# Kernel tuning notes

Measured on AMD Instinct MI355X. Metric: run time of the kernel, lower is better.

The kernel has to match this reference:

```python
import jax, jax.numpy as jnp
import numpy as np

B, F, S, H = 1024, 64, 512, 128


def setup_inputs() -> dict:
    key = jax.random.key(0)
    ks = jax.random.split(key, 9)
    x = jax.random.normal(ks[0], (B, F, S), dtype=jnp.float32)
    available_len = jax.random.randint(ks[1], (B,), 1, S // 2).astype(jnp.int32)
    extra = jax.random.randint(ks[2], (B,), 0, S // 2)
    predict_len = jnp.minimum(available_len + extra, S).astype(jnp.int32)
    s = 1.0 / float(np.sqrt(H))  # PyTorch default uniform init scale
    u = lambda k, shape: jax.random.uniform(k, shape, jnp.float32, -s, s)
    W_ih = u(ks[3], (4 * H, F))
    W_hh = u(ks[4], (4 * H, H))
    b_ih = u(ks[5], (4 * H,))
    b_hh = u(ks[6], (4 * H,))
    W_den = u(ks[7], (F, H))
    b_den = u(ks[8], (F,))
    init_ch = jnp.zeros((1, 2 * H), dtype=jnp.float32)  # nn.Parameter(zeros(1, 2*n_hidden))
    return {"x": x, "available_len": available_len, "predict_len": predict_len,
            "W_ih": W_ih, "W_hh": W_hh, "b_ih": b_ih, "b_hh": b_hh,
            "W_den": W_den, "b_den": b_den, "init_ch": init_ch}


def reference(x, available_len, predict_len, W_ih, W_hh, b_ih, b_hh, W_den, b_den, init_ch):
    """Masked autoregressive LSTMCell recurrence.

    Row r is active at step t iff t < predict_len[r]; once inactive it never
    re-activates (the torch code's per-step gather of c_1/h_1 by predict_len is
    exactly this monotone-shrinking active set, expressed here as a masked
    full-batch state update). For t >= available_len[r] (and still active) the
    input is the model's own previous prediction (auto-regression feedback).
    Returns the permuted buffer (seq_len, batch, n_fea), matching the torch code.
    """
    Bb, Ff, Ss = x.shape
    Hh = W_hh.shape[1]
    xs = jnp.transpose(x, (2, 0, 1))  # (S, B, F)
    c0 = jnp.broadcast_to(init_ch[:, :Hh], (Bb, Hh))
    h0 = jnp.broadcast_to(init_ch[:, Hh:], (Bb, Hh))

    def step(carry, inp):
        h, c, prev_out = carry
        t, x_t = inp  # t: scalar step index, x_t: (B, F)
        sel = t < predict_len                       # active rows
        use_pred = (t >= available_len) & sel
        inp_t = jnp.where(use_pred[:, None], prev_out, x_t)
        gates = inp_t @ W_ih.T + b_ih + h @ W_hh.T + b_hh  # (B, 4H)
        i, f, g, o = jnp.split(gates, 4, axis=-1)
        c_new = jax.nn.sigmoid(f) * c + jax.nn.sigmoid(i) * jnp.tanh(g)
        h_new = jax.nn.sigmoid(o) * jnp.tanh(c_new)
        h = jnp.where(sel[:, None], h_new, h)
        c = jnp.where(sel[:, None], c_new, c)
        pred = h_new @ W_den.T + b_den              # (B, F)
        out_t = jnp.where(sel[:, None], pred, inp_t)  # x[t, sel] <- prediction
        return (h, c, out_t), out_t

    _, ys = jax.lax.scan(step, (h0, c0, jnp.zeros_like(xs[0])),
                         (jnp.arange(Ss), xs))
    return ys  # (S, B, F)
```

## Files before the change

kernel.cpp:

```cpp
#include <hip/hip_runtime.h>

#define BB 1024
#define FF 64
#define SS 512
#define HH 128
#define ZP 200
#define ZROWS 16
#define OUTS (BB*FF)

typedef __attribute__((ext_vector_type(8))) short bf16x8;
typedef __attribute__((ext_vector_type(4))) float f32x4;

__device__ __forceinline__ unsigned short f2bf(float f) {
    unsigned int u = __float_as_uint(f);
    u += 0x7fff + ((u >> 16) & 1);
    return (unsigned short)(u >> 16);
}

__device__ __forceinline__ void bar_lds() {
    __builtin_amdgcn_sched_barrier(0);
    asm volatile("s_waitcnt lgkmcnt(0)\n\ts_barrier" ::: "memory");
    __builtin_amdgcn_sched_barrier(0);
}

__global__ void fold_kernel(const float* __restrict__ W_ih,
                            const float* __restrict__ W_den,
                            const float* __restrict__ b_den,
                            float* __restrict__ ws)
{
    const int n = blockIdx.x;
    const int k = threadIdx.x;
    float s = 0.f;
    #pragma unroll 8
    for (int f = 0; f < FF; ++f) s = fmaf(W_ih[n*FF + f], W_den[f*HH + k], s);
    ws[n*HH + k] = s;
    if (k == 0) {
        float bsum = 0.f;
        #pragma unroll 8
        for (int f = 0; f < FF; ++f) bsum = fmaf(W_ih[n*FF + f], b_den[f], bsum);
        ws[4*HH*HH + n] = bsum;
    }
}

__global__ __launch_bounds__(512)
void lstm_mfma_kernel(const float* __restrict__ x,
                      const int* __restrict__ available_len,
                      const int* __restrict__ predict_len,
                      const float* __restrict__ W_ih,
                      const float* __restrict__ W_hh,
                      const float* __restrict__ b_ih,
                      const float* __restrict__ b_hh,
                      const float* __restrict__ W_den,
                      const float* __restrict__ b_den,
                      const float* __restrict__ init_ch,
                      const float* __restrict__ ws,
                      float* __restrict__ out)
{
    const int b0  = blockIdx.x * 4;
    const int tid = threadIdx.x;
    const int w   = tid >> 6;
    const int l   = tid & 63;
    const int l16 = l & 15;
    const int lq  = l >> 4;
    const bool w4 = (w < 4);

    __shared__ __align__(16) unsigned short zbuf[2][ZROWS * ZP];

    for (int i = tid; i < 2 * ZROWS * ZP / 2; i += 512)
        ((unsigned int*)zbuf)[i] = 0u;

    const int p0 = predict_len[b0], p1 = predict_len[b0+1],
              p2 = predict_len[b0+2], p3 = predict_len[b0+3];
    const int a0i = available_len[b0], a1i = available_len[b0+1],
              a2i = available_len[b0+2], a3i = available_len[b0+3];
    const int maxP  = max(max(p0, p1), max(p2, p3));
    const int tsw   = max(max(a0i, a1i), max(a2i, a3i));
    const int P_my  = predict_len[b0 + lq];
    const int AV_my = available_len[b0 + lq];

    bf16x8 wg[4][6];
    float bias[4];
    #pragma unroll
    for (int g = 0; g < 4; ++g) {
        const int n = 128*g + 16*w + l16;
        const float* rih = W_ih + n * FF;
        const float* rhh = W_hh + n * HH;
        #pragma unroll
        for (int kt = 0; kt < 6; ++kt) {
            const int k = 32*kt + 8*lq;
            const float* src = (k < 64) ? (rih + k) : (rhh + (k - 64));
            bf16x8 r;
            #pragma unroll
            for (int i = 0; i < 8; i++) r[i] = (short)f2bf(src[i]);
            wg[g][kt] = r;
        }
        bias[g] = b_ih[n] + b_hh[n];
    }

    bf16x8 wd0, wd1, wd2, wd3;
    float bden = 0.f;
    size_t xbase = 0;
    int AV_x = 0;
    if (w4) {
        const int f = 16*w + l16;
        const float* rd = W_den + f * HH;
        bf16x8 r;
        #pragma unroll
        for (int i = 0; i < 8; i++) r[i] = (short)f2bf(rd[0*32 + 8*lq + i]);
        wd0 = r;
        #pragma unroll
        for (int i = 0; i < 8; i++) r[i] = (short)f2bf(rd[1*32 + 8*lq + i]);
        wd1 = r;
        #pragma unroll
        for (int i = 0; i < 8; i++) r[i] = (short)f2bf(rd[2*32 + 8*lq + i]);
        wd2 = r;
        #pragma unroll
        for (int i = 0; i < 8; i++) r[i] = (short)f2bf(rd[3*32 + 8*lq + i]);
        wd3 = r;
        bden = b_den[f];
        xbase = ((size_t)(b0 + w) * FF + l) * SS;
        AV_x  = available_len[b0 + w];
    }

    const int unit  = 16*w + l16;
    const int abase = l16*ZP + 8*lq;
    float c = init_ch[unit];
    const float h0v = init_ch[HH + unit];
    float* outb = out + (size_t)(b0 + lq) * FF + 16*w + l16;

    bar_lds();

    zbuf[0][(4*lq)*ZP + 64 + unit] = f2bf(h0v);
    if (w4) zbuf[0][(4*w)*ZP + l] = f2bf(x[xbase]);

    float4 qc = {0.f,0.f,0.f,0.f};
    if (w4 && AV_x > 1) qc = *(const float4*)(x + xbase);

    int cur = 0;

#define DO_STEP(S, XNEXT)                                                      \
  do {                                                                         \
    const int s_ = (S);                                                        \
    bar_lds();                                               \
    const unsigned short* zc_ = zbuf[cur];                                     \
    bf16x8 a0 = *(const bf16x8*)(zc_ + abase +   0);                           \
    bf16x8 a1 = *(const bf16x8*)(zc_ + abase +  32);                           \
    bf16x8 a2 = *(const bf16x8*)(zc_ + abase +  64);                           \
    bf16x8 a3 = *(const bf16x8*)(zc_ + abase +  96);                           \
    bf16x8 a4 = *(const bf16x8*)(zc_ + abase + 128);                           \
    bf16x8 a5 = *(const bf16x8*)(zc_ + abase + 160);                           \
    f32x4 ac0 = {0.f,0.f,0.f,0.f}, ac1 = {0.f,0.f,0.f,0.f},                    \
          ac2 = {0.f,0.f,0.f,0.f}, ac3 = {0.f,0.f,0.f,0.f};                    \
    ac0 = __builtin_amdgcn_mfma_f32_16x16x32_bf16(a0, wg[0][0], ac0, 0,0,0);   \
    ac1 = __builtin_amdgcn_mfma_f32_16x16x32_bf16(a0, wg[1][0], ac1, 0,0,0);   \
    ac2 = __builtin_amdgcn_mfma_f32_16x16x32_bf16(a0, wg[2][0], ac2, 0,0,0);   \
    ac3 = __builtin_amdgcn_mfma_f32_16x16x32_bf16(a0, wg[3][0], ac3, 0,0,0);   \
    ac0 = __builtin_amdgcn_mfma_f32_16x16x32_bf16(a1, wg[0][1], ac0, 0,0,0);   \
    ac1 = __builtin_amdgcn_mfma_f32_16x16x32_bf16(a1, wg[1][1], ac1, 0,0,0);   \
    ac2 = __builtin_amdgcn_mfma_f32_16x16x32_bf16(a1, wg[2][1], ac2, 0,0,0);   \
    ac3 = __builtin_amdgcn_mfma_f32_16x16x32_bf16(a1, wg[3][1], ac3, 0,0,0);   \
    ac0 = __builtin_amdgcn_mfma_f32_16x16x32_bf16(a2, wg[0][2], ac0, 0,0,0);   \
    ac1 = __builtin_amdgcn_mfma_f32_16x16x32_bf16(a2, wg[1][2], ac1, 0,0,0);   \
    ac2 = __builtin_amdgcn_mfma_f32_16x16x32_bf16(a2, wg[2][2], ac2, 0,0,0);   \
    ac3 = __builtin_amdgcn_mfma_f32_16x16x32_bf16(a2, wg[3][2], ac3, 0,0,0);   \
    ac0 = __builtin_amdgcn_mfma_f32_16x16x32_bf16(a3, wg[0][3], ac0, 0,0,0);   \
    ac1 = __builtin_amdgcn_mfma_f32_16x16x32_bf16(a3, wg[1][3], ac1, 0,0,0);   \
    ac2 = __builtin_amdgcn_mfma_f32_16x16x32_bf16(a3, wg[2][3], ac2, 0,0,0);   \
    ac3 = __builtin_amdgcn_mfma_f32_16x16x32_bf16(a3, wg[3][3], ac3, 0,0,0);   \
    ac0 = __builtin_amdgcn_mfma_f32_16x16x32_bf16(a4, wg[0][4], ac0, 0,0,0);   \
    ac1 = __builtin_amdgcn_mfma_f32_16x16x32_bf16(a4, wg[1][4], ac1, 0,0,0);   \
    ac2 = __builtin_amdgcn_mfma_f32_16x16x32_bf16(a4, wg[2][4], ac2, 0,0,0);   \
    ac3 = __builtin_amdgcn_mfma_f32_16x16x32_bf16(a4, wg[3][4], ac3, 0,0,0);   \
    ac0 = __builtin_amdgcn_mfma_f32_16x16x32_bf16(a5, wg[0][5], ac0, 0,0,0);   \
    ac1 = __builtin_amdgcn_mfma_f32_16x16x32_bf16(a5, wg[1][5], ac1, 0,0,0);   \
    ac2 = __builtin_amdgcn_mfma_f32_16x16x32_bf16(a5, wg[2][5], ac2, 0,0,0);   \
    ac3 = __builtin_amdgcn_mfma_f32_16x16x32_bf16(a5, wg[3][5], ac3, 0,0,0);   \
    const float g0 = ac0[0] + bias[0];                                         \
    const float g1 = ac1[0] + bias[1];                                         \
    const float g2 = ac2[0] + bias[2];                                         \
    const float g3 = ac3[0] + bias[3];                                         \
    const float si = 1.f / (1.f + __expf(-g0));                                \
    const float sf = 1.f / (1.f + __expf(-g1));                                \
    const float tg = 1.f - 2.f / (__expf(2.f * g2) + 1.f);                     \
    const float so = 1.f / (1.f + __expf(-g3));                                \
    const float cn = sf * c + si * tg;                                         \
    const float tc = 1.f - 2.f / (__expf(2.f * cn) + 1.f);                     \
    const float hn = so * tc;                                                  \
    const int nxt_ = cur ^ 1;                                                  \
    if (s_ < P_my) { c = cn; zbuf[nxt_][(4*lq)*ZP + 64 + unit] = f2bf(hn); }   \
    bar_lds();                                                \
    if (w4) {                                                                  \
      const unsigned short* zn_ = zbuf[nxt_];                                  \
      bf16x8 h0f = *(const bf16x8*)(zn_ + abase + 64 +  0);                    \
      bf16x8 h1f = *(const bf16x8*)(zn_ + abase + 64 + 32);                    \
      bf16x8 h2f = *(const bf16x8*)(zn_ + abase + 64 + 64);                    \
      bf16x8 h3f = *(const bf16x8*)(zn_ + abase + 64 + 96);                    \
      f32x4 pa = {0.f,0.f,0.f,0.f}, pb = {0.f,0.f,0.f,0.f};                    \
      pa = __builtin_amdgcn_mfma_f32_16x16x32_bf16(h0f, wd0, pa, 0,0,0);       \
      pb = __builtin_amdgcn_mfma_f32_16x16x32_bf16(h2f, wd2, pb, 0,0,0);       \
      pa = __builtin_amdgcn_mfma_f32_16x16x32_bf16(h1f, wd1, pa, 0,0,0);       \
      pb = __builtin_amdgcn_mfma_f32_16x16x32_bf16(h3f, wd3, pb, 0,0,0);       \
      const float pred_ = pa[0] + pb[0] + bden;                                \
      if (s_ < P_my) {                                                         \
        outb[(size_t)s_ * OUTS] = pred_;                                       \
        if (s_ + 1 >= AV_my)                                                   \
          zbuf[nxt_][(4*lq)*ZP + 16*w + l16] = f2bf(pred_);                    \
      }                                                                        \
      if (s_ + 1 < AV_x) zbuf[nxt_][(4*w)*ZP + l] = f2bf(XNEXT);               \
    }                                                                          \
    cur = nxt_;                                                                \
  } while (0)

    int t4 = 0;
    for (; t4 + 4 <= tsw; t4 += 4) {
        float4 qn = {0.f,0.f,0.f,0.f};
        if (w4 && (t4 + 4 < AV_x))
            qn = *(const float4*)(x + xbase + t4 + 4);
        DO_STEP(t4 + 0, qc.y);
        DO_STEP(t4 + 1, qc.z);
        DO_STEP(t4 + 2, qc.w);
        DO_STEP(t4 + 3, qn.x);
        qc = qn;
    }
    for (; t4 < tsw; ++t4) {
        float xs = 0.f;
        if (w4 && (t4 + 1 < AV_x)) xs = x[xbase + t4 + 1];
        DO_STEP(t4, xs);
    }
#undef DO_STEP

    if (tsw < maxP) {
        const float* wfold = ws;
        const float* bfold = ws + 4*HH*HH;
        #pragma unroll
        for (int g = 0; g < 4; ++g) {
            const int n = 128*g + 16*w + l16;
            const float* rhh = W_hh + n * HH;
            const float* rfo = wfold + n * HH;
            #pragma unroll
            for (int j = 0; j < 4; ++j) {
                const int k = 32*j + 8*lq;
                bf16x8 r;
                #pragma unroll
                for (int i = 0; i < 8; i++) r[i] = (short)f2bf(rhh[k+i] + rfo[k+i]);
                wg[g][j] = r;
            }
            bias[g] += bfold[n];
        }

        for (int t = tsw; t < maxP; ++t) {
            bar_lds();
            const unsigned short* zc = zbuf[cur];
            bf16x8 h0f = *(const bf16x8*)(zc + abase + 64 +  0);
            bf16x8 h1f = *(const bf16x8*)(zc + abase + 64 + 32);
            bf16x8 h2f = *(const bf16x8*)(zc + abase + 64 + 64);
            bf16x8 h3f = *(const bf16x8*)(zc + abase + 64 + 96);

            if (w4) {
                f32x4 pa = {0.f,0.f,0.f,0.f}, pb = {0.f,0.f,0.f,0.f};
                pa = __builtin_amdgcn_mfma_f32_16x16x32_bf16(h0f, wd0, pa, 0,0,0);
                pb = __builtin_amdgcn_mfma_f32_16x16x32_bf16(h2f, wd2, pb, 0,0,0);
                pa = __builtin_amdgcn_mfma_f32_16x16x32_bf16(h1f, wd1, pa, 0,0,0);
                pb = __builtin_amdgcn_mfma_f32_16x16x32_bf16(h3f, wd3, pb, 0,0,0);
                if (t > tsw && (t - 1) < P_my)
                    outb[(size_t)(t-1) * OUTS] = pa[0] + pb[0] + bden;
            }

            f32x4 ac0 = {0.f,0.f,0.f,0.f}, ac1 = {0.f,0.f,0.f,0.f},
                  ac2 = {0.f,0.f,0.f,0.f}, ac3 = {0.f,0.f,0.f,0.f};
            ac0 = __builtin_amdgcn_mfma_f32_16x16x32_bf16(h0f, wg[0][0], ac0, 0,0,0);
            ac1 = __builtin_amdgcn_mfma_f32_16x16x32_bf16(h0f, wg[1][0], ac1, 0,0,0);
            ac2 = __builtin_amdgcn_mfma_f32_16x16x32_bf16(h0f, wg[2][0], ac2, 0,0,0);
            ac3 = __builtin_amdgcn_mfma_f32_16x16x32_bf16(h0f, wg[3][0], ac3, 0,0,0);
            ac0 = __builtin_amdgcn_mfma_f32_16x16x32_bf16(h1f, wg[0][1], ac0, 0,0,0);
            ac1 = __builtin_amdgcn_mfma_f32_16x16x32_bf16(h1f, wg[1][1], ac1, 0,0,0);
            ac2 = __builtin_amdgcn_mfma_f32_16x16x32_bf16(h1f, wg[2][1], ac2, 0,0,0);
            ac3 = __builtin_amdgcn_mfma_f32_16x16x32_bf16(h1f, wg[3][1], ac3, 0,0,0);
            ac0 = __builtin_amdgcn_mfma_f32_16x16x32_bf16(h2f, wg[0][2], ac0, 0,0,0);
            ac1 = __builtin_amdgcn_mfma_f32_16x16x32_bf16(h2f, wg[1][2], ac1, 0,0,0);
            ac2 = __builtin_amdgcn_mfma_f32_16x16x32_bf16(h2f, wg[2][2], ac2, 0,0,0);
            ac3 = __builtin_amdgcn_mfma_f32_16x16x32_bf16(h2f, wg[3][2], ac3, 0,0,0);
            ac0 = __builtin_amdgcn_mfma_f32_16x16x32_bf16(h3f, wg[0][3], ac0, 0,0,0);
            ac1 = __builtin_amdgcn_mfma_f32_16x16x32_bf16(h3f, wg[1][3], ac1, 0,0,0);
            ac2 = __builtin_amdgcn_mfma_f32_16x16x32_bf16(h3f, wg[2][3], ac2, 0,0,0);
            ac3 = __builtin_amdgcn_mfma_f32_16x16x32_bf16(h3f, wg[3][3], ac3, 0,0,0);

            const float g0 = ac0[0] + bias[0];
            const float g1 = ac1[0] + bias[1];
            const float g2 = ac2[0] + bias[2];
            const float g3 = ac3[0] + bias[3];
            const float si = 1.f / (1.f + __expf(-g0));
            const float sf = 1.f / (1.f + __expf(-g1));
            const float tg = 1.f - 2.f / (__expf(2.f * g2) + 1.f);
            const float so = 1.f / (1.f + __expf(-g3));
            const float cn = sf * c + si * tg;
            const float tc = 1.f - 2.f / (__expf(2.f * cn) + 1.f);
            const float hn = so * tc;

            const int nxt = cur ^ 1;
            if (t < P_my) { c = cn; zbuf[nxt][(4*lq)*ZP + 64 + unit] = f2bf(hn); }
            cur = nxt;
        }

        bar_lds();
        if (w4) {
            const unsigned short* zc = zbuf[cur];
            bf16x8 h0f = *(const bf16x8*)(zc + abase + 64 +  0);
            bf16x8 h1f = *(const bf16x8*)(zc + abase + 64 + 32);
            bf16x8 h2f = *(const bf16x8*)(zc + abase + 64 + 64);
            bf16x8 h3f = *(const bf16x8*)(zc + abase + 64 + 96);
            f32x4 pa = {0.f,0.f,0.f,0.f}, pb = {0.f,0.f,0.f,0.f};
            pa = __builtin_amdgcn_mfma_f32_16x16x32_bf16(h0f, wd0, pa, 0,0,0);
            pb = __builtin_amdgcn_mfma_f32_16x16x32_bf16(h2f, wd2, pb, 0,0,0);
            pa = __builtin_amdgcn_mfma_f32_16x16x32_bf16(h1f, wd1, pa, 0,0,0);
            pb = __builtin_amdgcn_mfma_f32_16x16x32_bf16(h3f, wd3, pb, 0,0,0);
            if ((maxP - 1) < P_my)
                outb[(size_t)(maxP-1) * OUTS] = pa[0] + pb[0] + bden;
        }
    }
}

__global__ void tail_copy(const float* __restrict__ x,
                          const int* __restrict__ predict_len,
                          float* __restrict__ out)
{
    __shared__ float tile[64][65];
    const int b  = blockIdx.x;
    const int t0 = blockIdx.y * 64;
    const int P  = predict_len[b];
    if (t0 + 64 <= P) return;

    const int tid = threadIdx.x;
    const int tt  = tid & 63;
    const int fb  = tid >> 6;
    #pragma unroll
    for (int i = 0; i < 16; i++) {
        int f = fb * 16 + i;
        tile[f][tt] = x[(size_t)b * FF * SS + (size_t)f * SS + t0 + tt];
    }
    __syncthreads();
    const int f2 = tid & 63;
    const int tb = tid >> 6;
    #pragma unroll
    for (int i = 0; i < 16; i++) {
        int tloc = tb * 16 + i;
        int t    = t0 + tloc;
        if (t >= P) out[(size_t)t * BB * FF + (size_t)b * FF + f2] = tile[f2][tloc];
    }
}

extern "C" void kernel_launch(void* const* d_in, const int* in_sizes, int n_in,
                              void* d_out, int out_size, void* d_ws, size_t ws_size,
                              hipStream_t stream) {
    const float* x       = (const float*)d_in[0];
    const int*   avail   = (const int*)  d_in[1];
    const int*   plen    = (const int*)  d_in[2];
    const float* W_ih    = (const float*)d_in[3];
    const float* W_hh    = (const float*)d_in[4];
    const float* b_ih    = (const float*)d_in[5];
    const float* b_hh    = (const float*)d_in[6];
    const float* W_den   = (const float*)d_in[7];
    const float* b_den   = (const float*)d_in[8];
    const float* init_ch = (const float*)d_in[9];
    float*       out     = (float*)d_out;
    float*       ws      = (float*)d_ws;

    fold_kernel<<<dim3(4*HH), dim3(HH), 0, stream>>>(W_ih, W_den, b_den, ws);
    tail_copy<<<dim3(BB, SS/64), dim3(256), 0, stream>>>(x, plen, out);
    lstm_mfma_kernel<<<dim3(BB/4), dim3(512), 0, stream>>>(
        x, avail, plen, W_ih, W_hh, b_ih, b_hh, W_den, b_den, init_ch, ws, out);
}
```

Baseline: 444.9 us.

## Sort batch rows by available length so blocks group similar-length sequences

A new single-block kernel ranks rows by available_len to build a permutation. The LSTM kernel then handles 4 permuted rows per block, so each block's teacher-forced phase (up to max available_len) and its autoregressive phase line up more tightly and fewer masked steps are wasted. Prediction outputs are now written during the teacher-forced steps as well, through dense-projection MFMAs fused into each step. This adds a serial O(B^2) sort kernel, indirect row indexing and extra MFMAs per step in exchange for lower per-block step counts.

Measured after the change: 472.6 us. +6.2%, slower.

```diff
diff --git a/kernel.cpp b/kernel.cpp
--- a/kernel.cpp
+++ b/kernel.cpp
@@ -42,6 +42,18 @@
     }
 }
 
+__global__ void sort_kernel(const int* __restrict__ avail, int* __restrict__ perm)
+{
+    const int i = threadIdx.x;
+    const int key = avail[i];
+    int rank = 0;
+    for (int j = 0; j < BB; ++j) {
+        const int kj = avail[j];
+        rank += (kj < key) || (kj == key && j < i);
+    }
+    perm[rank] = i;
+}
+
 __global__ __launch_bounds__(512)
 void lstm_mfma_kernel(const float* __restrict__ x,
                       const int* __restrict__ available_len,
@@ -54,6 +66,7 @@
                       const float* __restrict__ b_den,
                       const float* __restrict__ init_ch,
                       const float* __restrict__ ws,
+                      const int* __restrict__ perm,
                       float* __restrict__ out)
 {
     const int b0  = blockIdx.x * 4;
@@ -69,14 +82,18 @@
     for (int i = tid; i < 2 * ZROWS * ZP / 2; i += 512)
         ((unsigned int*)zbuf)[i] = 0u;
 
-    const int p0 = predict_len[b0], p1 = predict_len[b0+1],
-              p2 = predict_len[b0+2], p3 = predict_len[b0+3];
-    const int a0i = available_len[b0], a1i = available_len[b0+1],
-              a2i = available_len[b0+2], a3i = available_len[b0+3];
+    const int rr0 = perm[b0], rr1 = perm[b0+1], rr2 = perm[b0+2], rr3 = perm[b0+3];
+    const int p0 = predict_len[rr0], p1 = predict_len[rr1],
+              p2 = predict_len[rr2], p3 = predict_len[rr3];
+    const int a0i = available_len[rr0], a1i = available_len[rr1],
+              a2i = available_len[rr2], a3i = available_len[rr3];
     const int maxP  = max(max(p0, p1), max(p2, p3));
     const int tsw   = max(max(a0i, a1i), max(a2i, a3i));
-    const int P_my  = predict_len[b0 + lq];
-    const int AV_my = available_len[b0 + lq];
+    const int tmin  = min(min(a0i, a1i), min(a2i, a3i));
+    const int ph1s  = (tmin > 1) ? (tmin - 1) : 0;
+    const int rl    = perm[b0 + lq];
+    const int P_my  = predict_len[rl];
+    const int AV_my = available_len[rl];
 
     bf16x8 wg[4][6];
     float bias[4];
@@ -118,15 +135,16 @@
         for (int i = 0; i < 8; i++) r[i] = (short)f2bf(rd[3*32 + 8*lq + i]);
         wd3 = r;
         bden = b_den[f];
-        xbase = ((size_t)(b0 + w) * FF + l) * SS;
-        AV_x  = available_len[b0 + w];
+        const int rx = perm[b0 + w];
+        xbase = ((size_t)rx * FF + l) * SS;
+        AV_x  = available_len[rx];
     }
 
     const int unit  = 16*w + l16;
     const int abase = l16*ZP + 8*lq;
     float c = init_ch[unit];
     const float h0v = init_ch[HH + unit];
-    float* outb = out + (size_t)(b0 + lq) * FF + 16*w + l16;
+    float* outb = out + (size_t)rl * FF + 16*w + l16;
 
     bar_lds();
 
@@ -134,9 +152,71 @@
     if (w4) zbuf[0][(4*w)*ZP + l] = f2bf(x[xbase]);
 
     float4 qc = {0.f,0.f,0.f,0.f};
-    if (w4 && AV_x > 1) qc = *(const float4*)(x + xbase);
+    if (AV_x > 1) qc = *(const float4*)(x + xbase);
 
     int cur = 0;
+
+#define DO_T(S, XNEXT)                                                         \
+  do {                                                                         \
+    const int s_ = (S);                                                        \
+    bar_lds();                                             \
+    const unsigned short* zc_ = zbuf[cur];                                     \
+    bf16x8 a0 = *(const bf16x8*)(zc_ + abase +   0);                           \
+    bf16x8 a1 = *(const bf16x8*)(zc_ + abase +  32);                           \
+    bf16x8 a2 = *(const bf16x8*)(zc_ + abase +  64);                           \
+    bf16x8 a3 = *(const bf16x8*)(zc_ + abase +  96);                           \
+    bf16x8 a4 = *(const bf16x8*)(zc_ + abase + 128);                           \
+    bf16x8 a5 = *(const bf16x8*)(zc_ + abase + 160);                           \
+    if (w4 && s_ >= 1) {                   \
+      f32x4 ca = {0.f,0.f,0.f,0.f}, cb = {0.f,0.f,0.f,0.f};                    \
+      ca = __builtin_amdgcn_mfma_f32_16x16x32_bf16(a2, wd0, ca, 0,0,0);        \
+      cb = __builtin_amdgcn_mfma_f32_16x16x32_bf16(a4, wd2, cb, 0,0,0);        \
+      ca = __builtin_amdgcn_mfma_f32_16x16x32_bf16(a3, wd1, ca, 0,0,0);        \
+      cb = __builtin_amdgcn_mfma_f32_16x16x32_bf16(a5, wd3, cb, 0,0,0);        \
+      if ((s_ - 1) < P_my) outb[(size_t)(s_-1) * OUTS] = ca[0] + cb[0] + bden; \
+    }                                                                          \
+    f32x4 ac0 = {0.f,0.f,0.f,0.f}, ac1 = {0.f,0.f,0.f,0.f},                    \
+          ac2 = {0.f,0.f,0.f,0.f}, ac3 = {0.f,0.f,0.f,0.f};                    \
+    ac0 = __builtin_amdgcn_mfma_f32_16x16x32_bf16(a0, wg[0][0], ac0, 0,0,0);   \
+    ac1 = __builtin_amdgcn_mfma_f32_16x16x32_bf16(a0, wg[1][0], ac1, 0,0,0);   \
+    ac2 = __builtin_amdgcn_mfma_f32_16x16x32_bf16(a0, wg[2][0], ac2, 0,0,0);   \
+    ac3 = __builtin_amdgcn_mfma_f32_16x16x32_bf16(a0, wg[3][0], ac3, 0,0,0);   \
+    ac0 = __builtin_amdgcn_mfma_f32_16x16x32_bf16(a1, wg[0][1], ac0, 0,0,0);   \
+    ac1 = __builtin_amdgcn_mfma_f32_16x16x32_bf16(a1, wg[1][1], ac1, 0,0,0);   \
+    ac2 = __builtin_amdgcn_mfma_f32_16x16x32_bf16(a1, wg[2][1], ac2, 0,0,0);   \
+    ac3 = __builtin_amdgcn_mfma_f32_16x16x32_bf16(a1, wg[3][1], ac3, 0,0,0);   \
+    ac0 = __builtin_amdgcn_mfma_f32_16x16x32_bf16(a2, wg[0][2], ac0, 0,0,0);   \
+    ac1 = __builtin_amdgcn_mfma_f32_16x16x32_bf16(a2, wg[1][2], ac1, 0,0,0);   \
+    ac2 = __builtin_amdgcn_mfma_f32_16x16x32_bf16(a2, wg[2][2], ac2, 0,0,0);   \
+    ac3 = __builtin_amdgcn_mfma_f32_16x16x32_bf16(a2, wg[3][2], ac3, 0,0,0);   \
+    ac0 = __builtin_amdgcn_mfma_f32_16x16x32_bf16(a3, wg[0][3], ac0, 0,0,0);   \
+    ac1 = __builtin_amdgcn_mfma_f32_16x16x32_bf16(a3, wg[1][3], ac1, 0,0,0);   \
+    ac2 = __builtin_amdgcn_mfma_f32_16x16x32_bf16(a3, wg[2][3], ac2, 0,0,0);   \
+    ac3 = __builtin_amdgcn_mfma_f32_16x16x32_bf16(a3, wg[3][3], ac3, 0,0,0);   \
+    ac0 = __builtin_amdgcn_mfma_f32_16x16x32_bf16(a4, wg[0][4], ac0, 0,0,0);   \
+    ac1 = __builtin_amdgcn_mfma_f32_16x16x32_bf16(a4, wg[1][4], ac1, 0,0,0);   \
+    ac2 = __builtin_amdgcn_mfma_f32_16x16x32_bf16(a4, wg[2][4], ac2, 0,0,0);   \
+    ac3 = __builtin_amdgcn_mfma_f32_16x16x32_bf16(a4, wg[3][4], ac3, 0,0,0);   \
+    ac0 = __builtin_amdgcn_mfma_f32_16x16x32_bf16(a5, wg[0][5], ac0, 0,0,0);   \
+    ac1 = __builtin_amdgcn_mfma_f32_16x16x32_bf16(a5, wg[1][5], ac1, 0,0,0);   \
+    ac2 = __builtin_amdgcn_mfma_f32_16x16x32_bf16(a5, wg[2][5], ac2, 0,0,0);   \
+    ac3 = __builtin_amdgcn_mfma_f32_16x16x32_bf16(a5, wg[3][5], ac3, 0,0,0);   \
+    const float g0 = ac0[0] + bias[0];                                         \
+    const float g1 = ac1[0] + bias[1];                                         \
+    const float g2 = ac2[0] + bias[2];                                         \
+    const float g3 = ac3[0] + bias[3];                                         \
+    const float si = 1.f / (1.f + __expf(-g0));                                \
+    const float sf = 1.f / (1.f + __expf(-g1));                                \
+    const float tg = 1.f - 2.f / (__expf(2.f * g2) + 1.f);                     \
+    const float so = 1.f / (1.f + __expf(-g3));                                \
+    const float cn = sf * c + si * tg;                                         \
+    const float tc = 1.f - 2.f / (__expf(2.f * cn) + 1.f);                     \
+    const float hn = so * tc;                                                  \
+    const int nxt_ = cur ^ 1;                                                  \
+    if (s_ < P_my) { c = cn; zbuf[nxt_][(4*lq)*ZP + 64 + unit] = f2bf(hn); }   \
+    if (w4 && (s_ + 1 < AV_x)) zbuf[nxt_][(4*w)*ZP + l] = f2bf(XNEXT);         \
+    cur = nxt_;                                                                \
+  } while (0)
 
 #define DO_STEP(S, XNEXT)                                                      \
   do {                                                                         \
@@ -149,6 +229,14 @@
     bf16x8 a3 = *(const bf16x8*)(zc_ + abase +  96);                           \
     bf16x8 a4 = *(const bf16x8*)(zc_ + abase + 128);                           \
     bf16x8 a5 = *(const bf16x8*)(zc_ + abase + 160);                           \
+    if (w4 && s_ >= 1) {                   \
+      f32x4 ca = {0.f,0.f,0.f,0.f}, cb = {0.f,0.f,0.f,0.f};                    \
+      ca = __builtin_amdgcn_mfma_f32_16x16x32_bf16(a2, wd0, ca, 0,0,0);        \
+      cb = __builtin_amdgcn_mfma_f32_16x16x32_bf16(a4, wd2, cb, 0,0,0);        \
+      ca = __builtin_amdgcn_mfma_f32_16x16x32_bf16(a3, wd1, ca, 0,0,0);        \
+      cb = __builtin_amdgcn_mfma_f32_16x16x32_bf16(a5, wd3, cb, 0,0,0);        \
+      if ((s_ - 1) < P_my) outb[(size_t)(s_-1) * OUTS] = ca[0] + cb[0] + bden; \
+    }                                                                          \
     f32x4 ac0 = {0.f,0.f,0.f,0.f}, ac1 = {0.f,0.f,0.f,0.f},                    \
           ac2 = {0.f,0.f,0.f,0.f}, ac3 = {0.f,0.f,0.f,0.f};                    \
     ac0 = __builtin_amdgcn_mfma_f32_16x16x32_bf16(a0, wg[0][0], ac0, 0,0,0);   \
@@ -212,21 +300,27 @@
   } while (0)
 
     int t4 = 0;
-    for (; t4 + 4 <= tsw; t4 += 4) {
+    for (; t4 + 4 <= ph1s; t4 += 4) {
         float4 qn = {0.f,0.f,0.f,0.f};
         if (w4 && (t4 + 4 < AV_x))
             qn = *(const float4*)(x + xbase + t4 + 4);
-        DO_STEP(t4 + 0, qc.y);
-        DO_STEP(t4 + 1, qc.z);
-        DO_STEP(t4 + 2, qc.w);
-        DO_STEP(t4 + 3, qn.x);
+        DO_T(t4 + 0, qc.y);
+        DO_T(t4 + 1, qc.z);
+        DO_T(t4 + 2, qc.w);
+        DO_T(t4 + 3, qn.x);
         qc = qn;
+    }
+    for (; t4 < ph1s; ++t4) {
+        float xs = 0.f;
+        if (w4 && (t4 + 1 < AV_x)) xs = x[xbase + t4 + 1];
+        DO_T(t4, xs);
     }
     for (; t4 < tsw; ++t4) {
         float xs = 0.f;
         if (w4 && (t4 + 1 < AV_x)) xs = x[xbase + t4 + 1];
         DO_STEP(t4, xs);
     }
+#undef DO_T
 #undef DO_STEP
 
     if (tsw < maxP) {
@@ -262,7 +356,7 @@
                 pb = __builtin_amdgcn_mfma_f32_16x16x32_bf16(h2f, wd2, pb, 0,0,0);
                 pa = __builtin_amdgcn_mfma_f32_16x16x32_bf16(h1f, wd1, pa, 0,0,0);
                 pb = __builtin_amdgcn_mfma_f32_16x16x32_bf16(h3f, wd3, pb, 0,0,0);
-                if (t > tsw && (t - 1) < P_my)
+                if ((t - 1) < P_my)
                     outb[(size_t)(t-1) * OUTS] = pa[0] + pb[0] + bden;
             }
 
@@ -364,9 +458,11 @@
     const float* init_ch = (const float*)d_in[9];
     float*       out     = (float*)d_out;
     float*       ws      = (float*)d_ws;
+    int*         perm    = (int*)(ws + 4*HH*HH + 4*HH);
 
     fold_kernel<<<dim3(4*HH), dim3(HH), 0, stream>>>(W_ih, W_den, b_den, ws);
+    sort_kernel<<<dim3(1), dim3(BB), 0, stream>>>(avail, perm);
     tail_copy<<<dim3(BB, SS/64), dim3(256), 0, stream>>>(x, plen, out);
     lstm_mfma_kernel<<<dim3(BB/4), dim3(512), 0, stream>>>(
-        x, avail, plen, W_ih, W_hh, b_ih, b_hh, W_den, b_den, init_ch, ws, out);
-}
+        x, avail, plen, W_ih, W_hh, b_ih, b_hh, W_den, b_den, init_ch, ws, perm, out);
+}
```
